# Kernel tuning notes

Hardware: AMD Instinct MI355X
Metric: run time of the kernel (lower is better)

The kernel has to match this reference:

```python
import jax, jax.numpy as jnp
import numpy as np

AREA = 4
NUM_HEADS = 4


def _conv1x1(x, w, s, t):
    # 1x1 Conv (bias=False) + folded BatchNorm: per-out-channel scale s, shift t
    y = jnp.einsum('bchw,oc->bohw', x, w)
    return y * s[None, :, None, None] + t[None, :, None, None]


def setup_inputs() -> dict:
    key = jax.random.key(0)
    ks = jax.random.split(key, 9)
    C, heads = 128, NUM_HEADS
    x = jax.random.normal(ks[0], (2, C, 80, 80), jnp.float32)

    def wmat(k, o, i):
        return jax.random.normal(k, (o, i), jnp.float32) * (i ** -0.5)

    def bn(k, n):
        k1, k2 = jax.random.split(k)
        s = 1.0 + 0.05 * jax.random.normal(k1, (n,), jnp.float32)
        t = 0.05 * jax.random.normal(k2, (n,), jnp.float32)
        return s, t

    w_qk = wmat(ks[1], 2 * C, C); s_qk, t_qk = bn(ks[2], 2 * C)
    w_in = wmat(ks[3], C, C); s_in, t_in = bn(ks[4], C)
    w_out = wmat(ks[5], C, C); s_out, t_out = bn(ks[6], C)
    w_fg = jax.random.normal(ks[7], (heads, heads, 1, 5), jnp.float32) * ((5 * heads) ** -0.5)
    s_fg, t_fg = bn(ks[8], heads)
    return dict(x=x, w_qk=w_qk, s_qk=s_qk, t_qk=t_qk, w_in=w_in, s_in=s_in,
                t_in=t_in, w_out=w_out, s_out=s_out, t_out=t_out,
                w_fg=w_fg, s_fg=s_fg, t_fg=t_fg)


def reference(x, w_qk, s_qk, t_qk, w_in, s_in, t_in, w_out, s_out, t_out, w_fg, s_fg, t_fg):
    B, C, H, W = x.shape
    N = H * W
    heads = NUM_HEADS
    hd = C // heads
    inp = x
    # qk projection -> [B, N, 2C]
    qk = _conv1x1(x, w_qk, s_qk, t_qk).reshape(B, 2 * C, N).transpose(0, 2, 1)
    # input-gated values -> [B, N, C]
    v = jax.nn.sigmoid(_conv1x1(x, w_in, s_in, t_in)) * x
    v = v.reshape(B, C, N).transpose(0, 2, 1)
    # area split
    Be, Na = B * AREA, N // AREA
    qk = qk.reshape(Be, Na, 2 * C)
    v = v.reshape(Be, Na, C)
    q, k = qk[..., :C], qk[..., C:]
    q = q.transpose(0, 2, 1).reshape(Be, heads, hd, Na)
    k = k.transpose(0, 2, 1).reshape(Be, heads, hd, Na)
    v = v.transpose(0, 2, 1).reshape(Be, heads, hd, Na)
    # full NxN attention per area/head
    attn = jnp.einsum('bhdn,bhdm->bhnm', q, k) * (hd ** -0.5)
    attn = jax.nn.softmax(attn, axis=-1)
    # forget gate: (1,5) conv mixing heads along last axis, pad (0,2), BN fold, SiLU
    attn = jax.lax.conv_general_dilated(attn, w_fg, (1, 1), ((0, 0), (2, 2)),
                                        dimension_numbers=('NCHW', 'OIHW', 'NCHW'))
    attn = attn * s_fg[None, :, None, None] + t_fg[None, :, None, None]
    attn = jax.nn.silu(attn)
    # v @ attn^T -> [Be, heads, hd, Na]
    o = jnp.einsum('bhdj,bhij->bhdi', v, attn)
    # merge areas back: [Be,Na,h,hd] -> [B,N,C] -> [B,C,H,W]
    o = o.transpose(0, 3, 1, 2).reshape(B, N, C)
    o = o.reshape(B, H, W, C).transpose(0, 3, 1, 2)
    return jax.nn.sigmoid(_conv1x1(o, w_out, s_out, t_out)) * o + inp
```

## Files before the change

### kernel.cpp

```cpp
#include <hip/hip_runtime.h>
#include <hip/hip_bf16.h>
#include <cstdint>

#define CC 128
#define NN 6400
#define NAa 1600
#define HEADS 4
#define HD 32
#define NB 16
#define MT 64

#define P_ROW 68
#define P_HEAD 1096
#define A_ROW 76
#define A_HEAD 1224

typedef __attribute__((ext_vector_type(8))) short bfrag8;
typedef __attribute__((ext_vector_type(4))) float ffrag4;
typedef union { uint2 u2[2]; bfrag8 f8; } cvt16;

#define LOG2E 1.4426950408889634f
#define QSCL (0.17677669529663687f * 1.4426950408889634f)

__device__ __forceinline__ float sigmoid_fast(float y) {
  return __builtin_amdgcn_rcpf(1.0f + __builtin_amdgcn_exp2f(-LOG2E * y));
}
__device__ __forceinline__ unsigned short f2bf(float f) {
  unsigned u = __float_as_uint(f);
  return (unsigned short)((u + 0x7FFFu + ((u >> 16) & 1u)) >> 16);
}
__device__ __forceinline__ unsigned pack_bf16(float a, float b) {
  return (unsigned)f2bf(a) | ((unsigned)f2bf(b) << 16);
}
__device__ __forceinline__ unsigned pk2(float a, float b) {
  float2 f2; f2.x = a; f2.y = b;
  __hip_bfloat162 h = __float22bfloat162_rn(f2);
  union { __hip_bfloat162 h2; unsigned u; } cv; cv.h2 = h;
  return cv.u;
}
__device__ __forceinline__ float bfl(unsigned u) { return __uint_as_float(u << 16); }
__device__ __forceinline__ float bfh(unsigned u) { return __uint_as_float(u & 0xFFFF0000u); }

__global__ __launch_bounds__(256) void prep_kernel(
    const float* __restrict__ x, const float* __restrict__ w_qk,
    const float* __restrict__ s_qk, const float* __restrict__ w_in,
    const float* __restrict__ s_in, const float* __restrict__ w_out,
    const float* __restrict__ s_out,
    unsigned short* __restrict__ xt, unsigned short* __restrict__ wqkb,
    unsigned short* __restrict__ wob) {
  __shared__ float tile[32][33];
  const int blk = blockIdx.x, tid = threadIdx.x;
  if (blk < 1600) {
    const int b = blk / 800, rem = blk - b * 800;
    const int ct = rem / 200, pt2 = rem - ct * 200;
    const int c0 = ct * 32, px0 = pt2 * 32;
    for (int i = tid; i < 1024; i += 256) {
      int r = i >> 5, p = i & 31;
      tile[r][p] = x[((size_t)(b * CC + c0 + r)) * NN + px0 + p];
    }
    __syncthreads();
    for (int i = tid; i < 512; i += 256) {
      int px = i >> 4, cp = i & 15;
      unsigned pk = pk2(tile[2 * cp][px], tile[2 * cp + 1][px]);
      *(unsigned*)&xt[((size_t)b * NN + px0 + px) * CC + c0 + 2 * cp] = pk;
    }
  } else if (blk < 1608) {
    const int r0 = (blk - 1600) * 48;
    for (int i = tid; i < 6144; i += 256) {
      int r = r0 + (i >> 7), c = i & 127;
      float wv, sv;
      if (r < 2 * CC) { wv = w_qk[r * CC + c]; sv = s_qk[r] * (r < CC ? QSCL : 1.0f); }
      else           { wv = w_in[(r - 2 * CC) * CC + c]; sv = s_in[r - 2 * CC]; }
      wqkb[r * CC + c] = f2bf(wv * sv);
    }
  } else {
    const int r0 = (blk - 1608) * 64;
    for (int i = tid; i < 8192; i += 256) {
      int r = r0 + (i >> 7), c = i & 127;
      wob[r * CC + c] = f2bf(w_out[r * CC + c] * s_out[r]);
    }
  }
}

__global__ __launch_bounds__(256) void qkv_kernel(
    const unsigned short* __restrict__ xt, const unsigned short* __restrict__ wqkb,
    const float* __restrict__ t_qk, const float* __restrict__ t_in,
    unsigned short* __restrict__ qt, unsigned short* __restrict__ kt,
    unsigned short* __restrict__ vb) {
  const int tid = threadIdx.x;
  const int w = tid >> 6, lane = tid & 63, lo = lane & 15, g = lane >> 4;
  const int blk = blockIdx.x;
  const int b = blk / 400, pt = blk - b * 400;
  const int ng0 = pt * 16;
  const int a = ng0 / NAa, na0 = ng0 - a * NAa;
  const int be = b * 4 + a;
  const size_t xrow = ((size_t)b * NN + ng0 + lo) * CC;
  bfrag8 bf[4];
#pragma unroll
  for (int kk = 0; kk < 4; kk++) bf[kk] = *(const bfrag8*)&xt[xrow + kk * 32 + g * 8];
#pragma unroll
  for (int mt6 = 0; mt6 < 6; mt6++) {
    const int rowbase = (w * 6 + mt6) * 16;
    ffrag4 d = {0.f, 0.f, 0.f, 0.f};
#pragma unroll
    for (int kk = 0; kk < 4; kk++) {
      bfrag8 af = *(const bfrag8*)&wqkb[(size_t)(rowbase + lo) * CC + kk * 32 + g * 8];
      d = __builtin_amdgcn_mfma_f32_16x16x32_bf16(af, bf[kk], d, 0, 0, 0);
    }
    const int r0c = rowbase + 4 * g;
    if (r0c < CC) {
      const int h = r0c >> 5, d0 = r0c & 31;
      uint2 pk;
      pk.x = pk2(d[0] + t_qk[r0c] * QSCL, d[1] + t_qk[r0c + 1] * QSCL);
      pk.y = pk2(d[2] + t_qk[r0c + 2] * QSCL, d[3] + t_qk[r0c + 3] * QSCL);
      *(uint2*)&qt[((size_t)(be * HEADS + h) * NAa + na0 + lo) * HD + d0] = pk;
    } else if (r0c < 2 * CC) {
      const int ch = r0c - CC, h = ch >> 5, d0 = ch & 31;
      uint2 pk;
      pk.x = pk2(d[0] + t_qk[r0c], d[1] + t_qk[r0c + 1]);
      pk.y = pk2(d[2] + t_qk[r0c + 2], d[3] + t_qk[r0c + 3]);
      *(uint2*)&kt[((size_t)(be * HEADS + h) * NAa + na0 + lo) * HD + d0] = pk;
    } else {
      const int ch0 = r0c - 2 * CC;
      const uint2 xv = *(const uint2*)&xt[xrow + ch0];
      float xr[4] = {bfl(xv.x), bfh(xv.x), bfl(xv.y), bfh(xv.y)};
#pragma unroll
      for (int r = 0; r < 4; r++) {
        float y = d[r] + t_in[ch0 + r];
        vb[((size_t)be * CC + ch0 + r) * NAa + na0 + lo] = f2bf(sigmoid_fast(y) * xr[r]);
      }
    }
  }
}

__global__ __launch_bounds__(256) void stats_kernel(
    const unsigned short* __restrict__ qt, const unsigned short* __restrict__ kt,
    float* __restrict__ pstats) {
  int tid = threadIdx.x;
  int h = tid >> 6, lane = tid & 63, lo = lane & 15, g = lane >> 4;
  int bid = blockIdx.x;
  int be = bid & 7;
  int rest = bid >> 3;
  int n0 = (rest % 100) * NB;
  int split = rest / 100;
  int ts0 = split ? 12 : 0, ts1 = split ? 25 : 12;

  const unsigned short* qtb = qt + (size_t)(be * HEADS + h) * NAa * HD;
  const unsigned short* ktb = kt + (size_t)(be * HEADS + h) * NAa * HD;

  bfrag8 qf = *(const bfrag8*)(qtb + (size_t)(n0 + lo) * HD + g * 8);
  float sm[4] = {0.f, 0.f, 0.f, 0.f};
  for (int t = ts0; t < ts1; t++) {
    int m0 = t * MT;
#pragma unroll
    for (int sb = 0; sb < 4; sb++) {
      bfrag8 kf = *(const bfrag8*)(ktb + (size_t)(m0 + sb * 16 + lo) * HD + g * 8);
      ffrag4 z = {0.f, 0.f, 0.f, 0.f};
      ffrag4 c = __builtin_amdgcn_mfma_f32_16x16x32_bf16(qf, kf, z, 0, 0, 0);
#pragma unroll
      for (int r = 0; r < 4; r++) sm[r] += __builtin_amdgcn_exp2f(c[r]);
    }
  }
#pragma unroll
  for (int r = 0; r < 4; r++) {
#pragma unroll
    for (int off = 1; off <= 8; off <<= 1) sm[r] += __shfl_xor(sm[r], off);
  }
  if (lo == 0) {
    float4 s4; s4.x = sm[0]; s4.y = sm[1]; s4.z = sm[2]; s4.w = sm[3];
    *(float4*)&pstats[((size_t)(split * 8 + be) * HEADS + h) * NAa + n0 + 4 * g] = s4;
  }
}

__global__ __launch_bounds__(512) void apply_kernel(
    const unsigned short* __restrict__ qt, const unsigned short* __restrict__ kt,
    const unsigned short* __restrict__ vb, const float* __restrict__ pstats,
    const float* __restrict__ w_fg, const float* __restrict__ s_fg,
    const float* __restrict__ t_fg, unsigned short* __restrict__ o_part) {
  __shared__ __align__(16) unsigned short Pb[2][HEADS * P_HEAD];
  __shared__ __align__(16) unsigned short A2s[HEADS * A_HEAD];
  const int tid = threadIdx.x;
  const int w = tid >> 6, lane = tid & 63, lo = lane & 15, g = lane >> 4;
  const int h = w >> 1, u = w & 1;
  const int bid = blockIdx.x;
  const int be = bid & 7;
  const int rest = bid >> 3;
  const int n0 = (rest % 100) * NB;
  const int split = rest / 100;
  const int ts0 = split ? 12 : 0;
  const int tend = split ? 26 : 12;

  const unsigned short* qtb = qt + (size_t)(be * HEADS + h) * NAa * HD;
  const unsigned short* ktb = kt + (size_t)(be * HEADS + h) * NAa * HD;
  const unsigned short* vhb = vb + (size_t)(be * CC + h * HD) * NAa;

  const bfrag8 qf = *(const bfrag8*)(qtb + (size_t)(n0 + lo) * HD + g * 8);

  bfrag8 wfrag;
  {
    const int ho = lo >> 2, s = lo & 3;
#pragma unroll
    for (int j = 0; j < 8; j++) {
      const int tp = j - s;
      float wv = (tp >= 0 && tp < 5) ? w_fg[(ho * HEADS + g) * 5 + tp] : 0.0f;
      wfrag[j] = (short)f2bf(wv);
    }
  }
  const float sfv = s_fg[g], tfv = t_fg[g];

  const float inv = 1.0f / (pstats[((size_t)(0 + be) * HEADS + h) * NAa + n0 + lo] +
                            pstats[((size_t)(8 + be) * HEADS + h) * NAa + n0 + lo]);

  ffrag4 oacc0 = {0.f, 0.f, 0.f, 0.f};
  ffrag4 oacc1 = {0.f, 0.f, 0.f, 0.f};

  unsigned short* P0 = Pb[0];
  if (split == 0) {
    if (u == 0 && g == 0) { uint2 zz; zz.x = 0; zz.y = 0; *(uint2*)&P0[h * P_HEAD + lo * P_ROW] = zz; }
  } else if (u == 0) {
    bfrag8 kf = *(const bfrag8*)(ktb + (size_t)(752 + lo) * HD + g * 8);
    ffrag4 z = {0.f, 0.f, 0.f, 0.f};
    ffrag4 c = __builtin_amdgcn_mfma_f32_16x16x32_bf16(kf, qf, z, 0, 0, 0);
    if (g == 3) {
      uint2 pk;
      pk.x = pk2(__builtin_amdgcn_exp2f(c[0]) * inv, __builtin_amdgcn_exp2f(c[1]) * inv);
      pk.y = pk2(__builtin_amdgcn_exp2f(c[2]) * inv, __builtin_amdgcn_exp2f(c[3]) * inv);
      *(uint2*)&P0[h * P_HEAD + lo * P_ROW] = pk;
    }
  }
  {
    const int m0 = ts0 * MT;
#pragma unroll
    for (int sbi = 0; sbi < 2; sbi++) {
      const int sb = 2 * u + sbi;
      bfrag8 kf = *(const bfrag8*)(ktb + (size_t)(m0 + sb * 16 + lo) * HD + g * 8);
      ffrag4 z = {0.f, 0.f, 0.f, 0.f};
      ffrag4 c = __builtin_amdgcn_mfma_f32_16x16x32_bf16(kf, qf, z, 0, 0, 0);
      uint2 pk;
      pk.x = pk2(__builtin_amdgcn_exp2f(c[0]) * inv, __builtin_amdgcn_exp2f(c[1]) * inv);
      pk.y = pk2(__builtin_amdgcn_exp2f(c[2]) * inv, __builtin_amdgcn_exp2f(c[3]) * inv);
      *(uint2*)&P0[h * P_HEAD + lo * P_ROW + 16 * sb + 4 * g + 4] = pk;
    }
  }
  __syncthreads();

  int cur = 0;
  for (int t = ts0; t < tend; t++) {
    const int m0 = t * MT;
    const bfrag8 vf0 = *(const bfrag8*)(vhb + (size_t)lo * NAa + (m0 - 2 + 32 * u + 8 * g));
    const bfrag8 vf1 = *(const bfrag8*)(vhb + (size_t)(16 + lo) * NAa + (m0 - 2 + 32 * u + 8 * g));
    const bool doqk = (t + 1 < tend);
    const bool realqk = doqk && (t + 1 < 25);
    bfrag8 kf0, kf1;
    if (realqk) {
      const int m1 = (t + 1) * MT;
      kf0 = *(const bfrag8*)(ktb + (size_t)(m1 + (2 * u) * 16 + lo) * HD + g * 8);
      kf1 = *(const bfrag8*)(ktb + (size_t)(m1 + (2 * u + 1) * 16 + lo) * HD + g * 8);
    }
    unsigned short* Pc = Pb[cur];
    unsigned short* Pn = Pb[cur ^ 1];
    if (doqk) {
      uint2 hh = *(const uint2*)&Pc[g * P_HEAD + lo * P_ROW + 64];
      *(uint2*)&Pn[g * P_HEAD + lo * P_ROW] = hh;
      if (realqk) {
        ffrag4 z = {0.f, 0.f, 0.f, 0.f};
        ffrag4 c0 = __builtin_amdgcn_mfma_f32_16x16x32_bf16(kf0, qf, z, 0, 0, 0);
        ffrag4 c1 = __builtin_amdgcn_mfma_f32_16x16x32_bf16(kf1, qf, z, 0, 0, 0);
        uint2 pk;
        pk.x = pk2(__builtin_amdgcn_exp2f(c0[0]) * inv, __builtin_amdgcn_exp2f(c0[1]) * inv);
        pk.y = pk2(__builtin_amdgcn_exp2f(c0[2]) * inv, __builtin_amdgcn_exp2f(c0[3]) * inv);
        *(uint2*)&Pn[h * P_HEAD + lo * P_ROW + 16 * (2 * u) + 4 * g + 4] = pk;
        pk.x = pk2(__builtin_amdgcn_exp2f(c1[0]) * inv, __builtin_amdgcn_exp2f(c1[1]) * inv);
        pk.y = pk2(__builtin_amdgcn_exp2f(c1[2]) * inv, __builtin_amdgcn_exp2f(c1[3]) * inv);
        *(uint2*)&Pn[h * P_HEAD + lo * P_ROW + 16 * (2 * u + 1) + 4 * g + 4] = pk;
      } else {
        uint2 zz; zz.x = 0; zz.y = 0;
        *(uint2*)&Pn[h * P_HEAD + lo * P_ROW + 16 * (2 * u) + 4 * g + 4] = zz;
        *(uint2*)&Pn[h * P_HEAD + lo * P_ROW + 16 * (2 * u + 1) + 4 * g + 4] = zz;
      }
    }
    const bool edge = (t == 0) || (t == 25);
#pragma unroll
    for (int ii = 0; ii < 2; ii++) {
      const int i = 2 * w + ii;
      cvt16 bb;
      bb.u2[0] = *(const uint2*)&Pc[g * P_HEAD + lo * P_ROW + 4 * i];
      bb.u2[1] = *(const uint2*)&Pc[g * P_HEAD + lo * P_ROW + 4 * i + 4];
      ffrag4 z = {0.f, 0.f, 0.f, 0.f};
      ffrag4 d = __builtin_amdgcn_mfma_f32_16x16x32_bf16(wfrag, bb.f8, z, 0, 0, 0);
      float a2v[4];
      if (edge) {
#pragma unroll
        for (int r = 0; r < 4; r++) {
          const int mp = m0 - 2 + 4 * i + r;
          float y = d[r] * sfv + tfv;
          float v = y * sigmoid_fast(y);
          a2v[r] = (mp >= 0 && mp < NAa) ? v : 0.0f;
        }
      } else {
#pragma unroll
        for (int r = 0; r < 4; r++) {
          float y = d[r] * sfv + tfv;
          a2v[r] = y * sigmoid_fast(y);
        }
      }
      uint2 pk;
      pk.x = pk2(a2v[0], a2v[1]);
      pk.y = pk2(a2v[2], a2v[3]);
      *(uint2*)&A2s[g * A_HEAD + lo * A_ROW + 4 * i] = pk;
    }
    __syncthreads();
    {
      cvt16 av;
      av.u2[0] = *(const uint2*)&A2s[h * A_HEAD + lo * A_ROW + 32 * u + 8 * g];
      av.u2[1] = *(const uint2*)&A2s[h * A_HEAD + lo * A_ROW + 32 * u + 8 * g + 4];
      oacc0 = __builtin_amdgcn_mfma_f32_16x16x32_bf16(av.f8, vf0, oacc0, 0, 0, 0);
      oacc1 = __builtin_amdgcn_mfma_f32_16x16x32_bf16(av.f8, vf1, oacc1, 0, 0, 0);
    }
    __syncthreads();
    cur ^= 1;
  }

  float* scr = (float*)A2s;
  if (u == 1) {
    float4 f0; f0.x = oacc0[0]; f0.y = oacc0[1]; f0.z = oacc0[2]; f0.w = oacc0[3];
    float4 f1; f1.x = oacc1[0]; f1.y = oacc1[1]; f1.z = oacc1[2]; f1.w = oacc1[3];
    *(float4*)&scr[(h * 64 + lane) * 8] = f0;
    *(float4*)&scr[(h * 64 + lane) * 8 + 4] = f1;
  }
  __syncthreads();
  if (u == 0) {
    const float4 f0 = *(const float4*)&scr[(h * 64 + lane) * 8];
    const float4 f1 = *(const float4*)&scr[(h * 64 + lane) * 8 + 4];
    const float fa[4] = {f0.x, f0.y, f0.z, f0.w};
    const float fb[4] = {f1.x, f1.y, f1.z, f1.w};
#pragma unroll
    for (int r = 0; r < 4; r++) {
      const size_t rowoff = ((size_t)(split * 8 + be) * NAa + n0 + 4 * g + r) * CC;
      o_part[rowoff + h * HD + lo] = f2bf(oacc0[r] + fa[r]);
      o_part[rowoff + h * HD + 16 + lo] = f2bf(oacc1[r] + fb[r]);
    }
  }
}

__global__ __launch_bounds__(256) void out_kernel(
    const unsigned short* __restrict__ o_part, const unsigned short* __restrict__ wob,
    const float* __restrict__ t_out, const float* __restrict__ x,
    float* __restrict__ out) {
  const int tid = threadIdx.x;
  const int w = tid >> 6, lane = tid & 63, lo = lane & 15, g = lane >> 4;
  const int blk = blockIdx.x;
  const int b = blk / 400, pt = blk - b * 400;
  const int ng0 = pt * 16;
  const int a = ng0 / NAa, na0 = ng0 - a * NAa;
  const int be = b * 4 + a;
  const size_t orow0 = ((size_t)(0 * 8 + be) * NAa + na0 + lo) * CC;
  const size_t orow1 = ((size_t)(1 * 8 + be) * NAa + na0 + lo) * CC;
  bfrag8 bf0[4], bf1[4];
#pragma unroll
  for (int kk = 0; kk < 4; kk++) {
    bf0[kk] = *(const bfrag8*)&o_part[orow0 + kk * 32 + g * 8];
    bf1[kk] = *(const bfrag8*)&o_part[orow1 + kk * 32 + g * 8];
  }
#pragma unroll
  for (int mt2 = 0; mt2 < 2; mt2++) {
    const int rowbase = (w * 2 + mt2) * 16;
    ffrag4 d = {0.f, 0.f, 0.f, 0.f};
#pragma unroll
    for (int kk = 0; kk < 4; kk++) {
      bfrag8 af = *(const bfrag8*)&wob[(size_t)(rowbase + lo) * CC + kk * 32 + g * 8];
      d = __builtin_amdgcn_mfma_f32_16x16x32_bf16(af, bf0[kk], d, 0, 0, 0);
      d = __builtin_amdgcn_mfma_f32_16x16x32_bf16(af, bf1[kk], d, 0, 0, 0);
    }
    const int ch0 = rowbase + 4 * g;
    const uint2 q0 = *(const uint2*)&o_part[orow0 + ch0];
    const uint2 q1 = *(const uint2*)&o_part[orow1 + ch0];
    float ov[4] = {bfl(q0.x) + bfl(q1.x), bfh(q0.x) + bfh(q1.x),
                   bfl(q0.y) + bfl(q1.y), bfh(q0.y) + bfh(q1.y)};
#pragma unroll
    for (int r = 0; r < 4; r++) {
      const size_t xi = ((size_t)b * CC + ch0 + r) * NN + ng0 + lo;
      float y = d[r] + t_out[ch0 + r];
      out[xi] = ov[r] * sigmoid_fast(y) + x[xi];
    }
  }
}

extern "C" void kernel_launch(void* const* d_in, const int* in_sizes, int n_in,
                              void* d_out, int out_size, void* d_ws, size_t ws_size,
                              hipStream_t stream) {
  const float* x    = (const float*)d_in[0];
  const float* w_qk = (const float*)d_in[1];
  const float* s_qk = (const float*)d_in[2];
  const float* t_qk = (const float*)d_in[3];
  const float* w_in = (const float*)d_in[4];
  const float* s_in = (const float*)d_in[5];
  const float* t_in = (const float*)d_in[6];
  const float* w_out = (const float*)d_in[7];
  const float* s_out = (const float*)d_in[8];
  const float* t_out = (const float*)d_in[9];
  const float* w_fg = (const float*)d_in[10];
  const float* s_fg = (const float*)d_in[11];
  const float* t_fg = (const float*)d_in[12];

  char* wsb = (char*)d_ws;
  unsigned short* o_part = (unsigned short*)wsb;
  unsigned short* vb_raw = (unsigned short*)(wsb + 6553600);
  unsigned short* vbp = vb_raw + 2;
  unsigned short* qt = (unsigned short*)(wsb + 9830464);
  unsigned short* kt = (unsigned short*)(wsb + 13107264);
  unsigned short* xt = (unsigned short*)(wsb + 16384064);
  unsigned short* wqkb = (unsigned short*)(wsb + 19660864);
  unsigned short* wob = (unsigned short*)(wsb + 19759168);
  float* pstats = (float*)(wsb + 19791936);
  float* out = (float*)d_out;

  prep_kernel<<<1610, 256, 0, stream>>>(x, w_qk, s_qk, w_in, s_in, w_out, s_out, xt, wqkb, wob);
  qkv_kernel<<<800, 256, 0, stream>>>(xt, wqkb, t_qk, t_in, qt, kt, vbp);
  stats_kernel<<<1600, 256, 0, stream>>>(qt, kt, pstats);
  apply_kernel<<<1600, 512, 0, stream>>>(qt, kt, vbp, pstats, w_fg, s_fg, t_fg, o_part);
  out_kernel<<<800, 256, 0, stream>>>(o_part, wob, t_out, x, out);
}
```

Measured before the change: 143.8 us.

## Restructure apply kernel so each wave owns all heads and a key range

The apply kernel moves from 512 threads, where waves split heads and key halves, to 128 threads, where each wave processes all four heads over its own half of the key tiles with a private LDS slab. This removes the two block-wide barriers per key tile. The softmax normalisation is folded into the MFMA accumulator as a log2 offset, which drops the per-element multiply. In exchange, register pressure rises sharply (q fragments, 16 K fragments, 16 V fragments and 8 accumulators per lane), and fewer waves are available per block for latency hiding.

```diff
diff --git a/kernel.cpp b/kernel.cpp
--- a/kernel.cpp
+++ b/kernel.cpp
@@ -14,6 +14,9 @@
 #define P_HEAD 1096
 #define A_ROW 76
 #define A_HEAD 1224
+#define PW (HEADS * P_HEAD)
+#define AW (HEADS * A_HEAD)
+#define WSLAB (PW + AW)
 
 typedef __attribute__((ext_vector_type(8))) short bfrag8;
 typedef __attribute__((ext_vector_type(4))) float ffrag4;
@@ -172,29 +175,34 @@
   }
 }
 
-__global__ __launch_bounds__(512) void apply_kernel(
+__global__ __launch_bounds__(128, 2) void apply_kernel(
     const unsigned short* __restrict__ qt, const unsigned short* __restrict__ kt,
     const unsigned short* __restrict__ vb, const float* __restrict__ pstats,
     const float* __restrict__ w_fg, const float* __restrict__ s_fg,
     const float* __restrict__ t_fg, unsigned short* __restrict__ o_part) {
-  __shared__ __align__(16) unsigned short Pb[2][HEADS * P_HEAD];
-  __shared__ __align__(16) unsigned short A2s[HEADS * A_HEAD];
+  __shared__ __align__(16) unsigned short lds[2 * WSLAB];
   const int tid = threadIdx.x;
   const int w = tid >> 6, lane = tid & 63, lo = lane & 15, g = lane >> 4;
-  const int h = w >> 1, u = w & 1;
   const int bid = blockIdx.x;
   const int be = bid & 7;
   const int rest = bid >> 3;
   const int n0 = (rest % 100) * NB;
   const int split = rest / 100;
-  const int ts0 = split ? 12 : 0;
-  const int tend = split ? 26 : 12;
-
-  const unsigned short* qtb = qt + (size_t)(be * HEADS + h) * NAa * HD;
-  const unsigned short* ktb = kt + (size_t)(be * HEADS + h) * NAa * HD;
-  const unsigned short* vhb = vb + (size_t)(be * CC + h * HD) * NAa;
-
-  const bfrag8 qf = *(const bfrag8*)(qtb + (size_t)(n0 + lo) * HD + g * 8);
+  const int bs = split * 13;
+  const int t0 = bs + (w ? 7 : 0);
+  const int t1 = bs + (w ? 13 : 7);
+
+  unsigned short* Pw_ = lds + w * WSLAB;
+  unsigned short* A2w = Pw_ + PW;
+
+  const unsigned short* qtb = qt + (size_t)(be * HEADS) * NAa * HD;
+  const unsigned short* ktb = kt + (size_t)(be * HEADS) * NAa * HD;
+  const unsigned short* vbb = vb + (size_t)be * CC * NAa;
+
+  bfrag8 qf[HEADS];
+#pragma unroll
+  for (int h = 0; h < HEADS; ++h)
+    qf[h] = *(const bfrag8*)(qtb + ((size_t)h * NAa + n0 + lo) * HD + g * 8);
 
   bfrag8 wfrag;
   {
@@ -208,90 +216,80 @@
   }
   const float sfv = s_fg[g], tfv = t_fg[g];
 
-  const float inv = 1.0f / (pstats[((size_t)(0 + be) * HEADS + h) * NAa + n0 + lo] +
-                            pstats[((size_t)(8 + be) * HEADS + h) * NAa + n0 + lo]);
-
-  ffrag4 oacc0 = {0.f, 0.f, 0.f, 0.f};
-  ffrag4 oacc1 = {0.f, 0.f, 0.f, 0.f};
-
-  unsigned short* P0 = Pb[0];
-  if (split == 0) {
-    if (u == 0 && g == 0) { uint2 zz; zz.x = 0; zz.y = 0; *(uint2*)&P0[h * P_HEAD + lo * P_ROW] = zz; }
-  } else if (u == 0) {
-    bfrag8 kf = *(const bfrag8*)(ktb + (size_t)(752 + lo) * HD + g * 8);
+  float linv[HEADS];
+#pragma unroll
+  for (int h = 0; h < HEADS; ++h) {
+    const float den = pstats[((size_t)(0 + be) * HEADS + h) * NAa + n0 + lo] +
+                      pstats[((size_t)(8 + be) * HEADS + h) * NAa + n0 + lo];
+    linv[h] = -__log2f(den);
+  }
+
+  if (t0 == 0) {
+    uint2 zz; zz.x = 0; zz.y = 0;
+    *(uint2*)&Pw_[g * P_HEAD + lo * P_ROW] = zz;
+  } else {
+    const int mh = t0 * MT - 16;
+#pragma unroll
+    for (int h = 0; h < HEADS; ++h) {
+      bfrag8 kf = *(const bfrag8*)(ktb + ((size_t)h * NAa + mh + lo) * HD + g * 8);
+      ffrag4 cin = {linv[h], linv[h], linv[h], linv[h]};
+      ffrag4 c = __builtin_amdgcn_mfma_f32_16x16x32_bf16(kf, qf[h], cin, 0, 0, 0);
+      if (g == 3) {
+        uint2 pk;
+        pk.x = pk2(__builtin_amdgcn_exp2f(c[0]), __builtin_amdgcn_exp2f(c[1]));
+        pk.y = pk2(__builtin_amdgcn_exp2f(c[2]), __builtin_amdgcn_exp2f(c[3]));
+        *(uint2*)&Pw_[h * P_HEAD + lo * P_ROW] = pk;
+      }
+    }
+  }
+  {
+    const int m1 = t0 * MT;
+#pragma unroll
+    for (int h = 0; h < HEADS; ++h) {
+      ffrag4 cin = {linv[h], linv[h], linv[h], linv[h]};
+#pragma unroll
+      for (int sb = 0; sb < 4; ++sb) {
+        bfrag8 kf = *(const bfrag8*)(ktb + ((size_t)h * NAa + m1 + 16 * sb + lo) * HD + g * 8);
+        ffrag4 c = __builtin_amdgcn_mfma_f32_16x16x32_bf16(kf, qf[h], cin, 0, 0, 0);
+        uint2 pk;
+        pk.x = pk2(__builtin_amdgcn_exp2f(c[0]), __builtin_amdgcn_exp2f(c[1]));
+        pk.y = pk2(__builtin_amdgcn_exp2f(c[2]), __builtin_amdgcn_exp2f(c[3]));
+        *(uint2*)&Pw_[h * P_HEAD + lo * P_ROW + 16 * sb + 4 * g + 4] = pk;
+      }
+    }
+  }
+
+  ffrag4 oacc[HEADS][2];
+#pragma unroll
+  for (int h = 0; h < HEADS; ++h) {
     ffrag4 z = {0.f, 0.f, 0.f, 0.f};
-    ffrag4 c = __builtin_amdgcn_mfma_f32_16x16x32_bf16(kf, qf, z, 0, 0, 0);
-    if (g == 3) {
-      uint2 pk;
-      pk.x = pk2(__builtin_amdgcn_exp2f(c[0]) * inv, __builtin_amdgcn_exp2f(c[1]) * inv);
-      pk.y = pk2(__builtin_amdgcn_exp2f(c[2]) * inv, __builtin_amdgcn_exp2f(c[3]) * inv);
-      *(uint2*)&P0[h * P_HEAD + lo * P_ROW] = pk;
-    }
-  }
-  {
-    const int m0 = ts0 * MT;
-#pragma unroll
-    for (int sbi = 0; sbi < 2; sbi++) {
-      const int sb = 2 * u + sbi;
-      bfrag8 kf = *(const bfrag8*)(ktb + (size_t)(m0 + sb * 16 + lo) * HD + g * 8);
-      ffrag4 z = {0.f, 0.f, 0.f, 0.f};
-      ffrag4 c = __builtin_amdgcn_mfma_f32_16x16x32_bf16(kf, qf, z, 0, 0, 0);
-      uint2 pk;
-      pk.x = pk2(__builtin_amdgcn_exp2f(c[0]) * inv, __builtin_amdgcn_exp2f(c[1]) * inv);
-      pk.y = pk2(__builtin_amdgcn_exp2f(c[2]) * inv, __builtin_amdgcn_exp2f(c[3]) * inv);
-      *(uint2*)&P0[h * P_HEAD + lo * P_ROW + 16 * sb + 4 * g + 4] = pk;
-    }
-  }
-  __syncthreads();
-
-  int cur = 0;
-  for (int t = ts0; t < tend; t++) {
+    oacc[h][0] = z; oacc[h][1] = z;
+  }
+
+  for (int t = t0; t < t1; ++t) {
     const int m0 = t * MT;
-    const bfrag8 vf0 = *(const bfrag8*)(vhb + (size_t)lo * NAa + (m0 - 2 + 32 * u + 8 * g));
-    const bfrag8 vf1 = *(const bfrag8*)(vhb + (size_t)(16 + lo) * NAa + (m0 - 2 + 32 * u + 8 * g));
-    const bool doqk = (t + 1 < tend);
-    const bool realqk = doqk && (t + 1 < 25);
-    bfrag8 kf0, kf1;
-    if (realqk) {
-      const int m1 = (t + 1) * MT;
-      kf0 = *(const bfrag8*)(ktb + (size_t)(m1 + (2 * u) * 16 + lo) * HD + g * 8);
-      kf1 = *(const bfrag8*)(ktb + (size_t)(m1 + (2 * u + 1) * 16 + lo) * HD + g * 8);
-    }
-    unsigned short* Pc = Pb[cur];
-    unsigned short* Pn = Pb[cur ^ 1];
-    if (doqk) {
-      uint2 hh = *(const uint2*)&Pc[g * P_HEAD + lo * P_ROW + 64];
-      *(uint2*)&Pn[g * P_HEAD + lo * P_ROW] = hh;
-      if (realqk) {
-        ffrag4 z = {0.f, 0.f, 0.f, 0.f};
-        ffrag4 c0 = __builtin_amdgcn_mfma_f32_16x16x32_bf16(kf0, qf, z, 0, 0, 0);
-        ffrag4 c1 = __builtin_amdgcn_mfma_f32_16x16x32_bf16(kf1, qf, z, 0, 0, 0);
-        uint2 pk;
-        pk.x = pk2(__builtin_amdgcn_exp2f(c0[0]) * inv, __builtin_amdgcn_exp2f(c0[1]) * inv);
-        pk.y = pk2(__builtin_amdgcn_exp2f(c0[2]) * inv, __builtin_amdgcn_exp2f(c0[3]) * inv);
-        *(uint2*)&Pn[h * P_HEAD + lo * P_ROW + 16 * (2 * u) + 4 * g + 4] = pk;
-        pk.x = pk2(__builtin_amdgcn_exp2f(c1[0]) * inv, __builtin_amdgcn_exp2f(c1[1]) * inv);
-        pk.y = pk2(__builtin_amdgcn_exp2f(c1[2]) * inv, __builtin_amdgcn_exp2f(c1[3]) * inv);
-        *(uint2*)&Pn[h * P_HEAD + lo * P_ROW + 16 * (2 * u + 1) + 4 * g + 4] = pk;
-      } else {
-        uint2 zz; zz.x = 0; zz.y = 0;
-        *(uint2*)&Pn[h * P_HEAD + lo * P_ROW + 16 * (2 * u) + 4 * g + 4] = zz;
-        *(uint2*)&Pn[h * P_HEAD + lo * P_ROW + 16 * (2 * u + 1) + 4 * g + 4] = zz;
+    bfrag8 vf[HEADS][2][2];
+#pragma unroll
+    for (int h = 0; h < HEADS; ++h) {
+      const unsigned short* vh = vbb + (size_t)(h * HD) * NAa;
+#pragma unroll
+      for (int u = 0; u < 2; ++u) {
+        vf[h][u][0] = *(const bfrag8*)(vh + (size_t)lo * NAa + (m0 - 2 + 32 * u + 8 * g));
+        vf[h][u][1] = *(const bfrag8*)(vh + (size_t)(16 + lo) * NAa + (m0 - 2 + 32 * u + 8 * g));
       }
     }
     const bool edge = (t == 0) || (t == 25);
 #pragma unroll
-    for (int ii = 0; ii < 2; ii++) {
-      const int i = 2 * w + ii;
+    for (int i = 0; i < 16; ++i) {
       cvt16 bb;
-      bb.u2[0] = *(const uint2*)&Pc[g * P_HEAD + lo * P_ROW + 4 * i];
-      bb.u2[1] = *(const uint2*)&Pc[g * P_HEAD + lo * P_ROW + 4 * i + 4];
+      bb.u2[0] = *(const uint2*)&Pw_[g * P_HEAD + lo * P_ROW + 4 * i];
+      bb.u2[1] = *(const uint2*)&Pw_[g * P_HEAD + lo * P_ROW + 4 * i + 4];
       ffrag4 z = {0.f, 0.f, 0.f, 0.f};
       ffrag4 d = __builtin_amdgcn_mfma_f32_16x16x32_bf16(wfrag, bb.f8, z, 0, 0, 0);
       float a2v[4];
       if (edge) {
 #pragma unroll
-        for (int r = 0; r < 4; r++) {
+        for (int r = 0; r < 4; ++r) {
           const int mp = m0 - 2 + 4 * i + r;
           float y = d[r] * sfv + tfv;
           float v = y * sigmoid_fast(y);
@@ -299,7 +297,7 @@
         }
       } else {
 #pragma unroll
-        for (int r = 0; r < 4; r++) {
+        for (int r = 0; r < 4; ++r) {
           float y = d[r] * sfv + tfv;
           a2v[r] = y * sigmoid_fast(y);
         }
@@ -307,38 +305,84 @@
       uint2 pk;
       pk.x = pk2(a2v[0], a2v[1]);
       pk.y = pk2(a2v[2], a2v[3]);
-      *(uint2*)&A2s[g * A_HEAD + lo * A_ROW + 4 * i] = pk;
-    }
-    __syncthreads();
-    {
-      cvt16 av;
-      av.u2[0] = *(const uint2*)&A2s[h * A_HEAD + lo * A_ROW + 32 * u + 8 * g];
-      av.u2[1] = *(const uint2*)&A2s[h * A_HEAD + lo * A_ROW + 32 * u + 8 * g + 4];
-      oacc0 = __builtin_amdgcn_mfma_f32_16x16x32_bf16(av.f8, vf0, oacc0, 0, 0, 0);
-      oacc1 = __builtin_amdgcn_mfma_f32_16x16x32_bf16(av.f8, vf1, oacc1, 0, 0, 0);
-    }
-    __syncthreads();
-    cur ^= 1;
-  }
-
-  float* scr = (float*)A2s;
-  if (u == 1) {
-    float4 f0; f0.x = oacc0[0]; f0.y = oacc0[1]; f0.z = oacc0[2]; f0.w = oacc0[3];
-    float4 f1; f1.x = oacc1[0]; f1.y = oacc1[1]; f1.z = oacc1[2]; f1.w = oacc1[3];
-    *(float4*)&scr[(h * 64 + lane) * 8] = f0;
-    *(float4*)&scr[(h * 64 + lane) * 8 + 4] = f1;
-  }
+      *(uint2*)&A2w[g * A_HEAD + lo * A_ROW + 4 * i] = pk;
+    }
+    const bool donext = (t + 1 < t1);
+    if (donext) {
+      uint2 hh = *(const uint2*)&Pw_[g * P_HEAD + lo * P_ROW + 64];
+      *(uint2*)&Pw_[g * P_HEAD + lo * P_ROW] = hh;
+    }
+    const bool realqk = donext && (t + 1 < 25);
+    bfrag8 kfp[HEADS][4];
+    if (realqk) {
+      const int m1 = (t + 1) * MT;
+#pragma unroll
+      for (int h = 0; h < HEADS; ++h)
+#pragma unroll
+        for (int sb = 0; sb < 4; ++sb)
+          kfp[h][sb] = *(const bfrag8*)(ktb + ((size_t)h * NAa + m1 + 16 * sb + lo) * HD + g * 8);
+    }
+#pragma unroll
+    for (int h = 0; h < HEADS; ++h) {
+#pragma unroll
+      for (int u = 0; u < 2; ++u) {
+        cvt16 av;
+        av.u2[0] = *(const uint2*)&A2w[h * A_HEAD + lo * A_ROW + 32 * u + 8 * g];
+        av.u2[1] = *(const uint2*)&A2w[h * A_HEAD + lo * A_ROW + 32 * u + 8 * g + 4];
+        oacc[h][0] = __builtin_amdgcn_mfma_f32_16x16x32_bf16(av.f8, vf[h][u][0], oacc[h][0], 0, 0, 0);
+        oacc[h][1] = __builtin_amdgcn_mfma_f32_16x16x32_bf16(av.f8, vf[h][u][1], oacc[h][1], 0, 0, 0);
+      }
+    }
+    if (donext) {
+      if (realqk) {
+#pragma unroll
+        for (int h = 0; h < HEADS; ++h) {
+          ffrag4 cin = {linv[h], linv[h], linv[h], linv[h]};
+#pragma unroll
+          for (int sb = 0; sb < 4; ++sb) {
+            ffrag4 c = __builtin_amdgcn_mfma_f32_16x16x32_bf16(kfp[h][sb], qf[h], cin, 0, 0, 0);
+            uint2 pk;
+            pk.x = pk2(__builtin_amdgcn_exp2f(c[0]), __builtin_amdgcn_exp2f(c[1]));
+            pk.y = pk2(__builtin_amdgcn_exp2f(c[2]), __builtin_amdgcn_exp2f(c[3]));
+            *(uint2*)&Pw_[h * P_HEAD + lo * P_ROW + 16 * sb + 4 * g + 4] = pk;
+          }
+        }
+      } else {
+        uint2 zz; zz.x = 0; zz.y = 0;
+#pragma unroll
+        for (int h = 0; h < HEADS; ++h)
+#pragma unroll
+          for (int sb = 0; sb < 4; ++sb)
+            *(uint2*)&Pw_[h * P_HEAD + lo * P_ROW + 16 * sb + 4 * g + 4] = zz;
+      }
+    }
+  }
+
   __syncthreads();
-  if (u == 0) {
-    const float4 f0 = *(const float4*)&scr[(h * 64 + lane) * 8];
-    const float4 f1 = *(const float4*)&scr[(h * 64 + lane) * 8 + 4];
-    const float fa[4] = {f0.x, f0.y, f0.z, f0.w};
-    const float fb[4] = {f1.x, f1.y, f1.z, f1.w};
-#pragma unroll
-    for (int r = 0; r < 4; r++) {
-      const size_t rowoff = ((size_t)(split * 8 + be) * NAa + n0 + 4 * g + r) * CC;
-      o_part[rowoff + h * HD + lo] = f2bf(oacc0[r] + fa[r]);
-      o_part[rowoff + h * HD + 16 + lo] = f2bf(oacc1[r] + fb[r]);
+  float* scrf = (float*)lds;
+  if (w == 1) {
+#pragma unroll
+    for (int h = 0; h < HEADS; ++h) {
+      float4 f0; f0.x = oacc[h][0][0]; f0.y = oacc[h][0][1]; f0.z = oacc[h][0][2]; f0.w = oacc[h][0][3];
+      float4 f1; f1.x = oacc[h][1][0]; f1.y = oacc[h][1][1]; f1.z = oacc[h][1][2]; f1.w = oacc[h][1][3];
+      *(float4*)&scrf[(h * 64 + lane) * 8] = f0;
+      *(float4*)&scrf[(h * 64 + lane) * 8 + 4] = f1;
+    }
+  }
+  __syncthreads();
+  if (w == 0) {
+#pragma unroll
+    for (int h = 0; h < HEADS; ++h) {
+      const float4 f0 = *(const float4*)&scrf[(h * 64 + lane) * 8];
+      const float4 f1 = *(const float4*)&scrf[(h * 64 + lane) * 8 + 4];
+      const float fa[4] = {f0.x, f0.y, f0.z, f0.w};
+      const float fb[4] = {f1.x, f1.y, f1.z, f1.w};
+#pragma unroll
+      for (int r = 0; r < 4; ++r) {
+        const size_t rowoff = ((size_t)(split * 8 + be) * NAa + n0 + 4 * g + r) * CC;
+        o_part[rowoff + h * HD + lo] = f2bf(oacc[h][0][r] + fa[r]);
+        o_part[rowoff + h * HD + 16 + lo] = f2bf(oacc[h][1][r] + fb[r]);
+      }
     }
   }
 }
@@ -418,6 +462,6 @@
   prep_kernel<<<1610, 256, 0, stream>>>(x, w_qk, s_qk, w_in, s_in, w_out, s_out, xt, wqkb, wob);
   qkv_kernel<<<800, 256, 0, stream>>>(xt, wqkb, t_qk, t_in, qt, kt, vbp);
   stats_kernel<<<1600, 256, 0, stream>>>(qt, kt, pstats);
-  apply_kernel<<<1600, 512, 0, stream>>>(qt, kt, vbp, pstats, w_fg, s_fg, t_fg, o_part);
+  apply_kernel<<<1600, 128, 0, stream>>>(qt, kt, vbp, pstats, w_fg, s_fg, t_fg, o_part);
   out_kernel<<<800, 256, 0, stream>>>(o_part, wob, t_out, x, out);
 }
```

Result: slower. 152.0 us (+5.7%).

## Process two query sub-tiles per apply block to reuse K and V fragments

Applied to the files above, without the earlier changes.

The apply kernel now handles 32 query rows per block as two 16-row sub-tiles, halving the grid to 800 blocks. Each loaded K fragment and V fragment feeds MFMAs for both sub-tiles, cutting global/L2 traffic for K/V and halving the per-tile barrier overhead. LDS use doubles (P double buffer and A2 scratch), and register pressure rises, which can lower occupancy. The stats kernel keeps its own 16-row tiling.

```diff
diff --git a/kernel.cpp b/kernel.cpp
--- a/kernel.cpp
+++ b/kernel.cpp
@@ -7,13 +7,15 @@
 #define NAa 1600
 #define HEADS 4
 #define HD 32
-#define NB 16
+#define NB 32
 #define MT 64
 
 #define P_ROW 68
 #define P_HEAD 1096
 #define A_ROW 76
 #define A_HEAD 1224
+#define PW (HEADS * P_HEAD)
+#define AW (HEADS * A_HEAD)
 
 typedef __attribute__((ext_vector_type(8))) short bfrag8;
 typedef __attribute__((ext_vector_type(4))) float ffrag4;
@@ -141,7 +143,7 @@
   int bid = blockIdx.x;
   int be = bid & 7;
   int rest = bid >> 3;
-  int n0 = (rest % 100) * NB;
+  int n0 = (rest % 100) * 16;
   int split = rest / 100;
   int ts0 = split ? 12 : 0, ts1 = split ? 25 : 12;
 
@@ -177,16 +179,16 @@
     const unsigned short* __restrict__ vb, const float* __restrict__ pstats,
     const float* __restrict__ w_fg, const float* __restrict__ s_fg,
     const float* __restrict__ t_fg, unsigned short* __restrict__ o_part) {
-  __shared__ __align__(16) unsigned short Pb[2][HEADS * P_HEAD];
-  __shared__ __align__(16) unsigned short A2s[HEADS * A_HEAD];
+  __shared__ __align__(16) unsigned short Pb[2][2 * PW];
+  __shared__ __align__(16) unsigned short A2s[2 * AW];
   const int tid = threadIdx.x;
   const int w = tid >> 6, lane = tid & 63, lo = lane & 15, g = lane >> 4;
   const int h = w >> 1, u = w & 1;
   const int bid = blockIdx.x;
   const int be = bid & 7;
   const int rest = bid >> 3;
-  const int n0 = (rest % 100) * NB;
-  const int split = rest / 100;
+  const int n0 = (rest % 50) * NB;
+  const int split = rest / 50;
   const int ts0 = split ? 12 : 0;
   const int tend = split ? 26 : 12;
 
@@ -194,7 +196,10 @@
   const unsigned short* ktb = kt + (size_t)(be * HEADS + h) * NAa * HD;
   const unsigned short* vhb = vb + (size_t)(be * CC + h * HD) * NAa;
 
-  const bfrag8 qf = *(const bfrag8*)(qtb + (size_t)(n0 + lo) * HD + g * 8);
+  bfrag8 qf[2];
+#pragma unroll
+  for (int qs = 0; qs < 2; ++qs)
+    qf[qs] = *(const bfrag8*)(qtb + (size_t)(n0 + 16 * qs + lo) * HD + g * 8);
 
   bfrag8 wfrag;
   {
@@ -208,24 +213,39 @@
   }
   const float sfv = s_fg[g], tfv = t_fg[g];
 
-  const float inv = 1.0f / (pstats[((size_t)(0 + be) * HEADS + h) * NAa + n0 + lo] +
-                            pstats[((size_t)(8 + be) * HEADS + h) * NAa + n0 + lo]);
-
-  ffrag4 oacc0 = {0.f, 0.f, 0.f, 0.f};
-  ffrag4 oacc1 = {0.f, 0.f, 0.f, 0.f};
+  float inv[2];
+#pragma unroll
+  for (int qs = 0; qs < 2; ++qs)
+    inv[qs] = 1.0f / (pstats[((size_t)(0 + be) * HEADS + h) * NAa + n0 + 16 * qs + lo] +
+                      pstats[((size_t)(8 + be) * HEADS + h) * NAa + n0 + 16 * qs + lo]);
+
+  ffrag4 oacc[2][2];
+#pragma unroll
+  for (int qs = 0; qs < 2; ++qs) {
+    ffrag4 z = {0.f, 0.f, 0.f, 0.f};
+    oacc[qs][0] = z; oacc[qs][1] = z;
+  }
 
   unsigned short* P0 = Pb[0];
   if (split == 0) {
-    if (u == 0 && g == 0) { uint2 zz; zz.x = 0; zz.y = 0; *(uint2*)&P0[h * P_HEAD + lo * P_ROW] = zz; }
+    if (u == 0 && g == 0) {
+      uint2 zz; zz.x = 0; zz.y = 0;
+#pragma unroll
+      for (int qs = 0; qs < 2; ++qs)
+        *(uint2*)&P0[qs * PW + h * P_HEAD + lo * P_ROW] = zz;
+    }
   } else if (u == 0) {
     bfrag8 kf = *(const bfrag8*)(ktb + (size_t)(752 + lo) * HD + g * 8);
-    ffrag4 z = {0.f, 0.f, 0.f, 0.f};
-    ffrag4 c = __builtin_amdgcn_mfma_f32_16x16x32_bf16(kf, qf, z, 0, 0, 0);
-    if (g == 3) {
-      uint2 pk;
-      pk.x = pk2(__builtin_amdgcn_exp2f(c[0]) * inv, __builtin_amdgcn_exp2f(c[1]) * inv);
-      pk.y = pk2(__builtin_amdgcn_exp2f(c[2]) * inv, __builtin_amdgcn_exp2f(c[3]) * inv);
-      *(uint2*)&P0[h * P_HEAD + lo * P_ROW] = pk;
+#pragma unroll
+    for (int qs = 0; qs < 2; ++qs) {
+      ffrag4 z = {0.f, 0.f, 0.f, 0.f};
+      ffrag4 c = __builtin_amdgcn_mfma_f32_16x16x32_bf16(kf, qf[qs], z, 0, 0, 0);
+      if (g == 3) {
+        uint2 pk;
+        pk.x = pk2(__builtin_amdgcn_exp2f(c[0]) * inv[qs], __builtin_amdgcn_exp2f(c[1]) * inv[qs]);
+        pk.y = pk2(__builtin_amdgcn_exp2f(c[2]) * inv[qs], __builtin_amdgcn_exp2f(c[3]) * inv[qs]);
+        *(uint2*)&P0[qs * PW + h * P_HEAD + lo * P_ROW] = pk;
+      }
     }
   }
   {
@@ -234,12 +254,15 @@
     for (int sbi = 0; sbi < 2; sbi++) {
       const int sb = 2 * u + sbi;
       bfrag8 kf = *(const bfrag8*)(ktb + (size_t)(m0 + sb * 16 + lo) * HD + g * 8);
-      ffrag4 z = {0.f, 0.f, 0.f, 0.f};
-      ffrag4 c = __builtin_amdgcn_mfma_f32_16x16x32_bf16(kf, qf, z, 0, 0, 0);
-      uint2 pk;
-      pk.x = pk2(__builtin_amdgcn_exp2f(c[0]) * inv, __builtin_amdgcn_exp2f(c[1]) * inv);
-      pk.y = pk2(__builtin_amdgcn_exp2f(c[2]) * inv, __builtin_amdgcn_exp2f(c[3]) * inv);
-      *(uint2*)&P0[h * P_HEAD + lo * P_ROW + 16 * sb + 4 * g + 4] = pk;
+#pragma unroll
+      for (int qs = 0; qs < 2; ++qs) {
+        ffrag4 z = {0.f, 0.f, 0.f, 0.f};
+        ffrag4 c = __builtin_amdgcn_mfma_f32_16x16x32_bf16(kf, qf[qs], z, 0, 0, 0);
+        uint2 pk;
+        pk.x = pk2(__builtin_amdgcn_exp2f(c[0]) * inv[qs], __builtin_amdgcn_exp2f(c[1]) * inv[qs]);
+        pk.y = pk2(__builtin_amdgcn_exp2f(c[2]) * inv[qs], __builtin_amdgcn_exp2f(c[3]) * inv[qs]);
+        *(uint2*)&P0[qs * PW + h * P_HEAD + lo * P_ROW + 16 * sb + 4 * g + 4] = pk;
+      }
     }
   }
   __syncthreads();
@@ -260,62 +283,75 @@
     unsigned short* Pc = Pb[cur];
     unsigned short* Pn = Pb[cur ^ 1];
     if (doqk) {
-      uint2 hh = *(const uint2*)&Pc[g * P_HEAD + lo * P_ROW + 64];
-      *(uint2*)&Pn[g * P_HEAD + lo * P_ROW] = hh;
+#pragma unroll
+      for (int qs = 0; qs < 2; ++qs) {
+        uint2 hh = *(const uint2*)&Pc[qs * PW + g * P_HEAD + lo * P_ROW + 64];
+        *(uint2*)&Pn[qs * PW + g * P_HEAD + lo * P_ROW] = hh;
+      }
       if (realqk) {
-        ffrag4 z = {0.f, 0.f, 0.f, 0.f};
-        ffrag4 c0 = __builtin_amdgcn_mfma_f32_16x16x32_bf16(kf0, qf, z, 0, 0, 0);
-        ffrag4 c1 = __builtin_amdgcn_mfma_f32_16x16x32_bf16(kf1, qf, z, 0, 0, 0);
-        uint2 pk;
-        pk.x = pk2(__builtin_amdgcn_exp2f(c0[0]) * inv, __builtin_amdgcn_exp2f(c0[1]) * inv);
-        pk.y = pk2(__builtin_amdgcn_exp2f(c0[2]) * inv, __builtin_amdgcn_exp2f(c0[3]) * inv);
-        *(uint2*)&Pn[h * P_HEAD + lo * P_ROW + 16 * (2 * u) + 4 * g + 4] = pk;
-        pk.x = pk2(__builtin_amdgcn_exp2f(c1[0]) * inv, __builtin_amdgcn_exp2f(c1[1]) * inv);
-        pk.y = pk2(__builtin_amdgcn_exp2f(c1[2]) * inv, __builtin_amdgcn_exp2f(c1[3]) * inv);
-        *(uint2*)&Pn[h * P_HEAD + lo * P_ROW + 16 * (2 * u + 1) + 4 * g + 4] = pk;
+#pragma unroll
+        for (int qs = 0; qs < 2; ++qs) {
+          ffrag4 z = {0.f, 0.f, 0.f, 0.f};
+          ffrag4 c0 = __builtin_amdgcn_mfma_f32_16x16x32_bf16(kf0, qf[qs], z, 0, 0, 0);
+          ffrag4 c1 = __builtin_amdgcn_mfma_f32_16x16x32_bf16(kf1, qf[qs], z, 0, 0, 0);
+          uint2 pk;
+          pk.x = pk2(__builtin_amdgcn_exp2f(c0[0]) * inv[qs], __builtin_amdgcn_exp2f(c0[1]) * inv[qs]);
+          pk.y = pk2(__builtin_amdgcn_exp2f(c0[2]) * inv[qs], __builtin_amdgcn_exp2f(c0[3]) * inv[qs]);
+          *(uint2*)&Pn[qs * PW + h * P_HEAD + lo * P_ROW + 16 * (2 * u) + 4 * g + 4] = pk;
+          pk.x = pk2(__builtin_amdgcn_exp2f(c1[0]) * inv[qs], __builtin_amdgcn_exp2f(c1[1]) * inv[qs]);
+          pk.y = pk2(__builtin_amdgcn_exp2f(c1[2]) * inv[qs], __builtin_amdgcn_exp2f(c1[3]) * inv[qs]);
+          *(uint2*)&Pn[qs * PW + h * P_HEAD + lo * P_ROW + 16 * (2 * u + 1) + 4 * g + 4] = pk;
+        }
       } else {
         uint2 zz; zz.x = 0; zz.y = 0;
-        *(uint2*)&Pn[h * P_HEAD + lo * P_ROW + 16 * (2 * u) + 4 * g + 4] = zz;
-        *(uint2*)&Pn[h * P_HEAD + lo * P_ROW + 16 * (2 * u + 1) + 4 * g + 4] = zz;
+#pragma unroll
+        for (int qs = 0; qs < 2; ++qs) {
+          *(uint2*)&Pn[qs * PW + h * P_HEAD + lo * P_ROW + 16 * (2 * u) + 4 * g + 4] = zz;
+          *(uint2*)&Pn[qs * PW + h * P_HEAD + lo * P_ROW + 16 * (2 * u + 1) + 4 * g + 4] = zz;
+        }
       }
     }
     const bool edge = (t == 0) || (t == 25);
 #pragma unroll
-    for (int ii = 0; ii < 2; ii++) {
-      const int i = 2 * w + ii;
-      cvt16 bb;
-      bb.u2[0] = *(const uint2*)&Pc[g * P_HEAD + lo * P_ROW + 4 * i];
-      bb.u2[1] = *(const uint2*)&Pc[g * P_HEAD + lo * P_ROW + 4 * i + 4];
-      ffrag4 z = {0.f, 0.f, 0.f, 0.f};
-      ffrag4 d = __builtin_amdgcn_mfma_f32_16x16x32_bf16(wfrag, bb.f8, z, 0, 0, 0);
-      float a2v[4];
-      if (edge) {
-#pragma unroll
-        for (int r = 0; r < 4; r++) {
-          const int mp = m0 - 2 + 4 * i + r;
-          float y = d[r] * sfv + tfv;
-          float v = y * sigmoid_fast(y);
-          a2v[r] = (mp >= 0 && mp < NAa) ? v : 0.0f;
+    for (int qs = 0; qs < 2; ++qs) {
+#pragma unroll
+      for (int ii = 0; ii < 2; ii++) {
+        const int i = 2 * w + ii;
+        cvt16 bb;
+        bb.u2[0] = *(const uint2*)&Pc[qs * PW + g * P_HEAD + lo * P_ROW + 4 * i];
+        bb.u2[1] = *(const uint2*)&Pc[qs * PW + g * P_HEAD + lo * P_ROW + 4 * i + 4];
+        ffrag4 z = {0.f, 0.f, 0.f, 0.f};
+        ffrag4 d = __builtin_amdgcn_mfma_f32_16x16x32_bf16(wfrag, bb.f8, z, 0, 0, 0);
+        float a2v[4];
+        if (edge) {
+#pragma unroll
+          for (int r = 0; r < 4; r++) {
+            const int mp = m0 - 2 + 4 * i + r;
+            float y = d[r] * sfv + tfv;
+            float v = y * sigmoid_fast(y);
+            a2v[r] = (mp >= 0 && mp < NAa) ? v : 0.0f;
+          }
+        } else {
+#pragma unroll
+          for (int r = 0; r < 4; r++) {
+            float y = d[r] * sfv + tfv;
+            a2v[r] = y * sigmoid_fast(y);
+          }
         }
-      } else {
-#pragma unroll
-        for (int r = 0; r < 4; r++) {
-          float y = d[r] * sfv + tfv;
-          a2v[r] = y * sigmoid_fast(y);
-        }
-      }
-      uint2 pk;
-      pk.x = pk2(a2v[0], a2v[1]);
-      pk.y = pk2(a2v[2], a2v[3]);
-      *(uint2*)&A2s[g * A_HEAD + lo * A_ROW + 4 * i] = pk;
+        uint2 pk;
+        pk.x = pk2(a2v[0], a2v[1]);
+        pk.y = pk2(a2v[2], a2v[3]);
+        *(uint2*)&A2s[qs * AW + g * A_HEAD + lo * A_ROW + 4 * i] = pk;
+      }
     }
     __syncthreads();
-    {
+#pragma unroll
+    for (int qs = 0; qs < 2; ++qs) {
       cvt16 av;
-      av.u2[0] = *(const uint2*)&A2s[h * A_HEAD + lo * A_ROW + 32 * u + 8 * g];
-      av.u2[1] = *(const uint2*)&A2s[h * A_HEAD + lo * A_ROW + 32 * u + 8 * g + 4];
-      oacc0 = __builtin_amdgcn_mfma_f32_16x16x32_bf16(av.f8, vf0, oacc0, 0, 0, 0);
-      oacc1 = __builtin_amdgcn_mfma_f32_16x16x32_bf16(av.f8, vf1, oacc1, 0, 0, 0);
+      av.u2[0] = *(const uint2*)&A2s[qs * AW + h * A_HEAD + lo * A_ROW + 32 * u + 8 * g];
+      av.u2[1] = *(const uint2*)&A2s[qs * AW + h * A_HEAD + lo * A_ROW + 32 * u + 8 * g + 4];
+      oacc[qs][0] = __builtin_amdgcn_mfma_f32_16x16x32_bf16(av.f8, vf0, oacc[qs][0], 0, 0, 0);
+      oacc[qs][1] = __builtin_amdgcn_mfma_f32_16x16x32_bf16(av.f8, vf1, oacc[qs][1], 0, 0, 0);
     }
     __syncthreads();
     cur ^= 1;
@@ -323,22 +359,28 @@
 
   float* scr = (float*)A2s;
   if (u == 1) {
-    float4 f0; f0.x = oacc0[0]; f0.y = oacc0[1]; f0.z = oacc0[2]; f0.w = oacc0[3];
-    float4 f1; f1.x = oacc1[0]; f1.y = oacc1[1]; f1.z = oacc1[2]; f1.w = oacc1[3];
-    *(float4*)&scr[(h * 64 + lane) * 8] = f0;
-    *(float4*)&scr[(h * 64 + lane) * 8 + 4] = f1;
+#pragma unroll
+    for (int qs = 0; qs < 2; ++qs) {
+      float4 f0; f0.x = oacc[qs][0][0]; f0.y = oacc[qs][0][1]; f0.z = oacc[qs][0][2]; f0.w = oacc[qs][0][3];
+      float4 f1; f1.x = oacc[qs][1][0]; f1.y = oacc[qs][1][1]; f1.z = oacc[qs][1][2]; f1.w = oacc[qs][1][3];
+      *(float4*)&scr[((qs * 4 + h) * 64 + lane) * 8] = f0;
+      *(float4*)&scr[((qs * 4 + h) * 64 + lane) * 8 + 4] = f1;
+    }
   }
   __syncthreads();
   if (u == 0) {
-    const float4 f0 = *(const float4*)&scr[(h * 64 + lane) * 8];
-    const float4 f1 = *(const float4*)&scr[(h * 64 + lane) * 8 + 4];
-    const float fa[4] = {f0.x, f0.y, f0.z, f0.w};
-    const float fb[4] = {f1.x, f1.y, f1.z, f1.w};
-#pragma unroll
-    for (int r = 0; r < 4; r++) {
-      const size_t rowoff = ((size_t)(split * 8 + be) * NAa + n0 + 4 * g + r) * CC;
-      o_part[rowoff + h * HD + lo] = f2bf(oacc0[r] + fa[r]);
-      o_part[rowoff + h * HD + 16 + lo] = f2bf(oacc1[r] + fb[r]);
+#pragma unroll
+    for (int qs = 0; qs < 2; ++qs) {
+      const float4 f0 = *(const float4*)&scr[((qs * 4 + h) * 64 + lane) * 8];
+      const float4 f1 = *(const float4*)&scr[((qs * 4 + h) * 64 + lane) * 8 + 4];
+      const float fa[4] = {f0.x, f0.y, f0.z, f0.w};
+      const float fb[4] = {f1.x, f1.y, f1.z, f1.w};
+#pragma unroll
+      for (int r = 0; r < 4; r++) {
+        const size_t rowoff = ((size_t)(split * 8 + be) * NAa + n0 + 16 * qs + 4 * g + r) * CC;
+        o_part[rowoff + h * HD + lo] = f2bf(oacc[qs][0][r] + fa[r]);
+        o_part[rowoff + h * HD + 16 + lo] = f2bf(oacc[qs][1][r] + fb[r]);
+      }
     }
   }
 }
@@ -418,6 +460,6 @@
   prep_kernel<<<1610, 256, 0, stream>>>(x, w_qk, s_qk, w_in, s_in, w_out, s_out, xt, wqkb, wob);
   qkv_kernel<<<800, 256, 0, stream>>>(xt, wqkb, t_qk, t_in, qt, kt, vbp);
   stats_kernel<<<1600, 256, 0, stream>>>(qt, kt, pstats);
-  apply_kernel<<<1600, 512, 0, stream>>>(qt, kt, vbp, pstats, w_fg, s_fg, t_fg, o_part);
+  apply_kernel<<<800, 512, 0, stream>>>(qt, kt, vbp, pstats, w_fg, s_fg, t_fg, o_part);
   out_kernel<<<800, 256, 0, stream>>>(o_part, wob, t_out, x, out);
 }
```

Result: no change. 142.0 us (-1.3%).
